# Kernel optimization log

Hardware: AMD Instinct MI355X
Metric: run time of the kernel (lower is better)

The kernel has to match this reference:

```python
import jax, jax.numpy as jnp
import numpy as np
from jax import lax


def _sobel_kernels(angle_deg, channel_n):
    dx = np.outer([1.0, 2.0, 1.0], [-1.0, 0.0, 1.0]) / 8.0
    dy = dx.T
    c = np.cos(angle_deg * np.pi / 180.0)
    s = np.sin(angle_deg * np.pi / 180.0)
    w1 = (c * dx - s * dy).astype(np.float32)
    w2 = (s * dx + c * dy).astype(np.float32)
    # depthwise kernels [C, 1, 3, 3] (OIHW with feature_group_count=C)
    k1 = jnp.tile(jnp.asarray(w1)[None, None], (channel_n, 1, 1, 1))
    k2 = jnp.tile(jnp.asarray(w2)[None, None], (channel_n, 1, 1, 1))
    return k1, k2


def _dwconv(x, k, groups):
    return lax.conv_general_dilated(
        x, k, window_strides=(1, 1), padding=[(1, 1), (1, 1)],
        feature_group_count=groups,
        dimension_numbers=('NCHW', 'OIHW', 'NCHW'))


def _maxpool3(x):
    # 3x3 max pool, stride 1, pad 1 over last two dims of NCHW
    return lax.reduce_window(x, -jnp.inf, lax.max,
                             (1, 1, 3, 3), (1, 1, 1, 1),
                             [(0, 0), (0, 0), (1, 1), (1, 1)])


def _alive(x_nchw):
    return _maxpool3(x_nchw[:, 3:4]) > 0.1


def _update(x, key, w0, b0, w1, wfr, k1, k2):
    # x: [B, H, W, C]  (torch does transpose(1,3) -> [B, C, W, H])
    xc = jnp.swapaxes(x, 1, 3)
    pre = _alive(xc)                               # [B,1,W,H] bool
    cn = xc.shape[1]
    y1 = _dwconv(xc, k1, cn)
    y2 = _dwconv(xc, k2, cn)
    dx = jnp.swapaxes(jnp.concatenate([xc, y1, y2], axis=1), 1, 3)  # [B,H,W,3C]
    fr = jax.nn.sigmoid(dx @ wfr.T) * jnp.swapaxes(pre, 1, 3)       # [B,H,W,1]
    log_fr = jnp.log(jnp.concatenate([fr, 1.0 - fr], axis=-1) + 1e-10)
    h = jax.nn.relu(dx @ w0.T + b0) @ w1.T                           # [B,H,W,C]
    # gumbel-softmax, tau=1, hard=True (straight-through)
    u = jax.random.uniform(key, log_fr.shape)
    g = -jnp.log(-jnp.log(u + 1e-20) + 1e-20)
    soft = jax.nn.softmax(log_fr + g, axis=-1)
    hard = jax.nn.one_hot(jnp.argmax(soft, axis=-1), 2, dtype=soft.dtype)
    update_grid = (hard + soft - lax.stop_gradient(soft))[..., 0:1]
    h = h * update_grid
    xc = xc + jnp.swapaxes(h, 1, 3)
    post = _alive(xc)
    xc = xc * (pre & post).astype(xc.dtype)
    return jnp.swapaxes(xc, 1, 3), fr[..., 0]


def setup_inputs() -> dict:
    key = jax.random.key(0)
    k = jax.random.split(key, 5)
    B, H, W, C, HID = 16, 128, 128, 16, 256
    return {
        'x': jax.random.uniform(k[0], (B, H, W, C), dtype=jnp.float32),
        'w0': jax.random.normal(k[1], (HID, 3 * C), dtype=jnp.float32) * 0.1,
        'b0': jax.random.normal(k[2], (HID,), dtype=jnp.float32) * 0.01,
        'w1': jax.random.normal(k[3], (C, HID), dtype=jnp.float32) * 0.1,
        'wfr': jax.random.normal(k[4], (1, 3 * C), dtype=jnp.float32) * 0.1,
        'steps': 4,
    }


def reference(x, w0, b0, w1, wfr, steps):
    angle = 0.0
    k1, k2 = _sobel_kernels(angle, x.shape[-1])
    keys = jax.random.split(jax.random.key(42), steps)

    def step(carry, key):
        xn, fr = _update(carry, key, w0, b0, w1, wfr, k1, k2)
        return xn, (xn, fr)

    _, (x_steps, fr_steps) = lax.scan(step, x, keys)
    return x_steps, fr_steps
```

## Files before the change

kernel.cpp:

```cpp
#include <hip/hip_runtime.h>
#include <cstdint>
#include <math.h>

#define HW2    16384
#define BHW    262144
#define XSLICE 4194304

__host__ __device__ static inline uint32_t rotl32(uint32_t v, int r) {
  return (v << r) | (v >> (32 - r));
}

__host__ __device__ static inline void tf2x32(uint32_t k0, uint32_t k1,
                                              uint32_t x0, uint32_t x1,
                                              uint32_t& o0, uint32_t& o1) {
  uint32_t ks2 = k0 ^ k1 ^ 0x1BD11BDAu;
  x0 += k0; x1 += k1;
#define TFR(r) { x0 += x1; x1 = rotl32(x1, (r)); x1 ^= x0; }
  TFR(13) TFR(15) TFR(26) TFR(6)   x0 += k1;  x1 += ks2 + 1u;
  TFR(17) TFR(29) TFR(16) TFR(24)  x0 += ks2; x1 += k0 + 2u;
  TFR(13) TFR(15) TFR(26) TFR(6)   x0 += k0;  x1 += k1 + 3u;
  TFR(17) TFR(29) TFR(16) TFR(24)  x0 += k1;  x1 += ks2 + 4u;
  TFR(13) TFR(15) TFR(26) TFR(6)   x0 += ks2; x1 += k0 + 5u;
#undef TFR
  o0 = x0; o1 = x1;
}

__device__ static inline float bits_to_unit(uint32_t bits) {
  return __uint_as_float((bits >> 9) | 0x3f800000u) - 1.0f;
}

__device__ static inline uint32_t rng_bits(uint32_t sk0, uint32_t sk1, uint32_t f) {
  uint32_t o0, o1;
  tf2x32(sk0, sk1, 0u, f, o0, o1);
  return o0 ^ o1;
}

__device__ static inline float sigmoidf_(float z) {
  if (z >= 0.f) { float e = expf(-z); return 1.f / (1.f + e); }
  float e = expf(z); return e / (1.f + e);
}

__device__ static inline void sobel_feat(const float* __restrict__ base,
                                         int hh, int ww, float* dxv, float& m3) {
#pragma unroll
  for (int c = 0; c < 48; ++c) dxv[c] = 0.f;
  m3 = -INFINITY;
#pragma unroll
  for (int dh = -1; dh <= 1; ++dh) {
    const int j = dh + 1;
    const int h2 = hh + dh;
    const bool hok = ((unsigned)h2 < 128u);
#pragma unroll
    for (int dw = -1; dw <= 1; ++dw) {
      const int i = dw + 1;
      const int w2 = ww + dw;
      float v[16];
      if (hok && ((unsigned)w2 < 128u)) {
        const float* s = base + (((h2 << 7) + w2) << 4);
#pragma unroll
        for (int c = 0; c < 16; c += 4) {
          float4 q = *(const float4*)(s + c);
          v[c] = q.x; v[c + 1] = q.y; v[c + 2] = q.z; v[c + 3] = q.w;
        }
        m3 = fmaxf(m3, v[3]);
      } else {
#pragma unroll
        for (int c = 0; c < 16; ++c) v[c] = 0.f;
      }
      const float smv[3] = {1.f, 2.f, 1.f};
      const float dfv[3] = {-1.f, 0.f, 1.f};
      const float c1 = smv[i] * dfv[j] * 0.125f;
      const float c2 = dfv[i] * smv[j] * 0.125f;
      if (dh == 0 && dw == 0) {
#pragma unroll
        for (int c = 0; c < 16; ++c) dxv[c] = v[c];
      }
      if (c1 != 0.f) {
#pragma unroll
        for (int c = 0; c < 16; ++c) dxv[16 + c] = fmaf(c1, v[c], dxv[16 + c]);
      }
      if (c2 != 0.f) {
#pragma unroll
        for (int c = 0; c < 16; ++c) dxv[32 + c] = fmaf(c2, v[c], dxv[32 + c]);
      }
    }
  }
}

__global__ __launch_bounds__(256, 2) void ca_step_a(
    const float* __restrict__ xin,
    const float* __restrict__ pw,
    const float* __restrict__ wfrg,
    float* __restrict__ xmid,
    float* __restrict__ ch3,
    float* __restrict__ premask,
    float* __restrict__ frout,
    uint32_t sk0, uint32_t sk1) {
  __shared__ float sw[128 * 68];

  const int tid = threadIdx.x;
  {
    const float4* src = (const float4*)pw;
    float4* dst = (float4*)sw;
    for (int i = tid; i < 2176; i += 256) dst[i] = src[i];
  }
  __syncthreads();

  const int p0  = blockIdx.x * 512 + tid;
  const int p1  = p0 + 256;
  const int b   = p0 >> 14;
  const int rem = p0 & 16383;
  const int hh0 = rem >> 7;
  const int ww0 = rem & 127;
  const int hh1 = hh0 + 2;

  const float* base = xin + ((size_t)b << 18);

  float dx0[48], dx1[48];
  float m30, m31;
  sobel_feat(base, hh0, ww0, dx0, m30);
  sobel_feat(base, hh1, ww0, dx1, m31);

  const bool pre0 = (m30 > 0.1f);
  const bool pre1 = (m31 > 0.1f);

  float z0 = 0.f, z1 = 0.f;
#pragma unroll
  for (int c = 0; c < 48; ++c) {
    z0 = fmaf(dx0[c], wfrg[c], z0);
    z1 = fmaf(dx1[c], wfrg[c], z1);
  }
  const float fr0 = pre0 ? sigmoidf_(z0) : 0.f;
  const float fr1 = pre1 ? sigmoidf_(z1) : 0.f;

  float upd0, upd1;
  {
    const float u0 = bits_to_unit(rng_bits(sk0, sk1, 2u * (uint32_t)p0));
    const float u1 = bits_to_unit(rng_bits(sk0, sk1, 2u * (uint32_t)p0 + 1u));
    const float d0 = logf(fr0 + 1e-10f) - logf(-logf(u0 + 1e-20f) + 1e-20f);
    const float d1 = logf(1.0f - fr0 + 1e-10f) - logf(-logf(u1 + 1e-20f) + 1e-20f);
    upd0 = (d0 >= d1) ? 1.f : 0.f;
  }
  {
    const float u0 = bits_to_unit(rng_bits(sk0, sk1, 2u * (uint32_t)p1));
    const float u1 = bits_to_unit(rng_bits(sk0, sk1, 2u * (uint32_t)p1 + 1u));
    const float d0 = logf(fr1 + 1e-10f) - logf(-logf(u0 + 1e-20f) + 1e-20f);
    const float d1 = logf(1.0f - fr1 + 1e-10f) - logf(-logf(u1 + 1e-20f) + 1e-20f);
    upd1 = (d0 >= d1) ? 1.f : 0.f;
  }

  float h0[16], h1[16];
#pragma unroll
  for (int c = 0; c < 16; ++c) { h0[c] = 0.f; h1[c] = 0.f; }

  for (int i = 0; i < 128; ++i) {
    const float* __restrict__ srow = pw + (size_t)(128 + i) * 68;
    float S[65];
#pragma unroll
    for (int q = 0; q < 65; ++q) S[q] = srow[q];

    {
      const float* row = sw + i * 68;
      float a00 = 0.f, a01 = 0.f, a10 = 0.f, a11 = 0.f;
#pragma unroll
      for (int ks = 0; ks < 6; ++ks) {
        const int k = ks * 8;
        const float4 wa = *(const float4*)(row + k);
        const float4 wb = *(const float4*)(row + k + 4);
        a00 = fmaf(wa.x, dx0[k + 0], a00); a01 = fmaf(wa.y, dx0[k + 1], a01);
        a00 = fmaf(wa.z, dx0[k + 2], a00); a01 = fmaf(wa.w, dx0[k + 3], a01);
        a00 = fmaf(wb.x, dx0[k + 4], a00); a01 = fmaf(wb.y, dx0[k + 5], a01);
        a00 = fmaf(wb.z, dx0[k + 6], a00); a01 = fmaf(wb.w, dx0[k + 7], a01);
        a10 = fmaf(wa.x, dx1[k + 0], a10); a11 = fmaf(wa.y, dx1[k + 1], a11);
        a10 = fmaf(wa.z, dx1[k + 2], a10); a11 = fmaf(wa.w, dx1[k + 3], a11);
        a10 = fmaf(wb.x, dx1[k + 4], a10); a11 = fmaf(wb.y, dx1[k + 5], a11);
        a10 = fmaf(wb.z, dx1[k + 6], a10); a11 = fmaf(wb.w, dx1[k + 7], a11);
      }
      const float bb = row[64];
      const float r0 = fmaxf(bb + (a00 + a01), 0.f);
      const float r1 = fmaxf(bb + (a10 + a11), 0.f);
#pragma unroll
      for (int c4 = 0; c4 < 4; ++c4) {
        const float4 q = *(const float4*)(row + 48 + (c4 << 2));
        const int c = c4 << 2;
        h0[c]     = fmaf(q.x, r0, h0[c]);     h1[c]     = fmaf(q.x, r1, h1[c]);
        h0[c + 1] = fmaf(q.y, r0, h0[c + 1]); h1[c + 1] = fmaf(q.y, r1, h1[c + 1]);
        h0[c + 2] = fmaf(q.z, r0, h0[c + 2]); h1[c + 2] = fmaf(q.z, r1, h1[c + 2]);
        h0[c + 3] = fmaf(q.w, r0, h0[c + 3]); h1[c + 3] = fmaf(q.w, r1, h1[c + 3]);
      }
    }

    {
      float a00 = 0.f, a01 = 0.f, a10 = 0.f, a11 = 0.f;
#pragma unroll
      for (int k = 0; k < 48; k += 2) {
        a00 = fmaf(S[k], dx0[k], a00);     a01 = fmaf(S[k + 1], dx0[k + 1], a01);
        a10 = fmaf(S[k], dx1[k], a10);     a11 = fmaf(S[k + 1], dx1[k + 1], a11);
      }
      const float bb = S[64];
      const float r0 = fmaxf(bb + (a00 + a01), 0.f);
      const float r1 = fmaxf(bb + (a10 + a11), 0.f);
#pragma unroll
      for (int c = 0; c < 16; ++c) {
        h0[c] = fmaf(S[48 + c], r0, h0[c]);
        h1[c] = fmaf(S[48 + c], r1, h1[c]);
      }
    }
  }

  float* dst0 = xmid + ((size_t)p0 << 4);
  float* dst1 = xmid + ((size_t)p1 << 4);
#pragma unroll
  for (int c = 0; c < 16; c += 4) {
    float4 q0, q1;
    q0.x = fmaf(upd0, h0[c],     dx0[c]);     q1.x = fmaf(upd1, h1[c],     dx1[c]);
    q0.y = fmaf(upd0, h0[c + 1], dx0[c + 1]); q1.y = fmaf(upd1, h1[c + 1], dx1[c + 1]);
    q0.z = fmaf(upd0, h0[c + 2], dx0[c + 2]); q1.z = fmaf(upd1, h1[c + 2], dx1[c + 2]);
    q0.w = fmaf(upd0, h0[c + 3], dx0[c + 3]); q1.w = fmaf(upd1, h1[c + 3], dx1[c + 3]);
    *(float4*)(dst0 + c) = q0;
    *(float4*)(dst1 + c) = q1;
  }
  ch3[p0]     = fmaf(upd0, h0[3], dx0[3]);
  ch3[p1]     = fmaf(upd1, h1[3], dx1[3]);
  premask[p0] = pre0 ? 1.f : 0.f;
  premask[p1] = pre1 ? 1.f : 0.f;
  frout[p0]   = fr0;
  frout[p1]   = fr1;
}

__global__ __launch_bounds__(256) void ca_step_b(
    float* __restrict__ xs, const float* __restrict__ ch3,
    const float* __restrict__ premask) {
  const int p   = blockIdx.x * 256 + threadIdx.x;
  const int b   = p >> 14;
  const int rem = p & 16383;
  const int hh  = rem >> 7;
  const int ww  = rem & 127;
  const float* cb = ch3 + (b << 14);
  float m = -INFINITY;
#pragma unroll
  for (int dh = -1; dh <= 1; ++dh) {
    const int h2 = hh + dh;
    if ((unsigned)h2 >= 128u) continue;
#pragma unroll
    for (int dw = -1; dw <= 1; ++dw) {
      const int w2 = ww + dw;
      if ((unsigned)w2 >= 128u) continue;
      m = fmaxf(m, cb[(h2 << 7) + w2]);
    }
  }
  const bool alive = (premask[p] != 0.f) && (m > 0.1f);
  if (!alive) {
    float4 z; z.x = 0.f; z.y = 0.f; z.z = 0.f; z.w = 0.f;
    float* dst = xs + ((size_t)p << 4);
    *(float4*)(dst)      = z;
    *(float4*)(dst + 4)  = z;
    *(float4*)(dst + 8)  = z;
    *(float4*)(dst + 12) = z;
  }
}

__global__ void pack_weights(const float* __restrict__ w0,
                             const float* __restrict__ b0,
                             const float* __restrict__ w1,
                             float* __restrict__ pw) {
  const int j = blockIdx.x * 256 + threadIdx.x;
  if (j < 256) {
    float* r = pw + j * 68;
#pragma unroll
    for (int k = 0; k < 48; ++k) r[k] = w0[j * 48 + k];
#pragma unroll
    for (int c = 0; c < 16; ++c) r[48 + c] = w1[c * 256 + j];
    r[64] = b0[j];
    r[65] = 0.f; r[66] = 0.f; r[67] = 0.f;
  }
}

extern "C" void kernel_launch(void* const* d_in, const int* in_sizes, int n_in,
                              void* d_out, int out_size, void* d_ws, size_t ws_size,
                              hipStream_t stream) {
  const float* x0  = (const float*)d_in[0];
  const float* w0  = (const float*)d_in[1];
  const float* b0  = (const float*)d_in[2];
  const float* w1  = (const float*)d_in[3];
  const float* wfr = (const float*)d_in[4];
  const int steps = 4;

  float* xsteps  = (float*)d_out;
  float* frsteps = xsteps + (size_t)steps * XSLICE;

  float* pw  = (float*)d_ws;
  float* ch3 = pw + 17408;
  float* pre = ch3 + BHW;

  uint32_t sk[4][2];
  for (int s = 0; s < steps; ++s)
    tf2x32(0u, 42u, 0u, (uint32_t)s, sk[s][0], sk[s][1]);

  pack_weights<<<1, 256, 0, stream>>>(w0, b0, w1, pw);
  for (int s = 0; s < steps; ++s) {
    const float* xin = (s == 0) ? x0 : (xsteps + (size_t)(s - 1) * XSLICE);
    float* xmid = xsteps + (size_t)s * XSLICE;
    ca_step_a<<<512, 256, 0, stream>>>(xin, pw, wfr, xmid, ch3, pre,
                                       frsteps + (size_t)s * BHW, sk[s][0], sk[s][1]);
    ca_step_b<<<1024, 256, 0, stream>>>(xmid, ch3, pre);
  }
}
```

Before: 462.8 us.

## Compact updating cells into a list and run the MLP only on them

Splits the step kernel into a gate kernel and an MLP kernel. The gate kernel computes the perception features, fire rate and Gumbel decision, writes the un-updated state, and appends the indices of updating cells to a list through an atomic counter. The MLP kernel then runs the hidden layer only over the compacted list, so cells with no update skip the 256-wide MLP. The price is an extra launch, recomputing Sobel features in the second kernel, gather-style scattered access, and nondeterministic list order from the atomics.

```diff
diff --git a/kernel.cpp b/kernel.cpp
--- a/kernel.cpp
+++ b/kernel.cpp
@@ -87,17 +87,67 @@
   }
 }
 
-__global__ __launch_bounds__(256, 2) void ca_step_a(
+__global__ __launch_bounds__(256) void ca_gate(
     const float* __restrict__ xin,
-    const float* __restrict__ pw,
     const float* __restrict__ wfrg,
     float* __restrict__ xmid,
     float* __restrict__ ch3,
     float* __restrict__ premask,
     float* __restrict__ frout,
+    int* __restrict__ list,
+    int* __restrict__ counter,
     uint32_t sk0, uint32_t sk1) {
+  const int p   = blockIdx.x * 256 + threadIdx.x;
+  const int b   = p >> 14;
+  const int rem = p & 16383;
+  const int hh  = rem >> 7;
+  const int ww  = rem & 127;
+
+  const float* base = xin + ((size_t)b << 18);
+  float dxv[48];
+  float m3;
+  sobel_feat(base, hh, ww, dxv, m3);
+  const bool pre = (m3 > 0.1f);
+
+  float z = 0.f;
+#pragma unroll
+  for (int c = 0; c < 48; ++c) z = fmaf(dxv[c], wfrg[c], z);
+  const float fr = pre ? sigmoidf_(z) : 0.f;
+
+  const float u0 = bits_to_unit(rng_bits(sk0, sk1, 2u * (uint32_t)p));
+  const float u1 = bits_to_unit(rng_bits(sk0, sk1, 2u * (uint32_t)p + 1u));
+  const float d0 = logf(fr + 1e-10f) - logf(-logf(u0 + 1e-20f) + 1e-20f);
+  const float d1 = logf(1.0f - fr + 1e-10f) - logf(-logf(u1 + 1e-20f) + 1e-20f);
+  const bool updb = (d0 >= d1);
+
+  float* dst = xmid + ((size_t)p << 4);
+#pragma unroll
+  for (int c = 0; c < 16; c += 4) {
+    float4 q;
+    q.x = dxv[c]; q.y = dxv[c + 1]; q.z = dxv[c + 2]; q.w = dxv[c + 3];
+    *(float4*)(dst + c) = q;
+  }
+  ch3[p]     = dxv[3];
+  premask[p] = pre ? 1.f : 0.f;
+  frout[p]   = fr;
+  if (updb) {
+    const int slot = atomicAdd(counter, 1);
+    list[slot] = p;
+  }
+}
+
+__global__ __launch_bounds__(256, 2) void ca_mlp(
+    const float* __restrict__ xin,
+    const float* __restrict__ pw,
+    const int* __restrict__ list,
+    const int* __restrict__ counter,
+    float* __restrict__ xmid,
+    float* __restrict__ ch3) {
+  const int count = *counter;
+  const int chunk = blockIdx.x * 512;
+  if (chunk >= count) return;
+
   __shared__ float sw[128 * 68];
-
   const int tid = threadIdx.x;
   {
     const float4* src = (const float4*)pw;
@@ -106,47 +156,22 @@
   }
   __syncthreads();
 
-  const int p0  = blockIdx.x * 512 + tid;
-  const int p1  = p0 + 256;
-  const int b   = p0 >> 14;
-  const int rem = p0 & 16383;
-  const int hh0 = rem >> 7;
-  const int ww0 = rem & 127;
-  const int hh1 = hh0 + 2;
-
-  const float* base = xin + ((size_t)b << 18);
+  const int e0 = chunk + tid;
+  const int e1 = e0 + 256;
+  const bool v0 = (e0 < count);
+  const bool v1 = (e1 < count);
+  const int p0 = v0 ? list[e0] : list[0];
+  const int p1 = v1 ? list[e1] : list[0];
 
   float dx0[48], dx1[48];
   float m30, m31;
-  sobel_feat(base, hh0, ww0, dx0, m30);
-  sobel_feat(base, hh1, ww0, dx1, m31);
-
-  const bool pre0 = (m30 > 0.1f);
-  const bool pre1 = (m31 > 0.1f);
-
-  float z0 = 0.f, z1 = 0.f;
-#pragma unroll
-  for (int c = 0; c < 48; ++c) {
-    z0 = fmaf(dx0[c], wfrg[c], z0);
-    z1 = fmaf(dx1[c], wfrg[c], z1);
-  }
-  const float fr0 = pre0 ? sigmoidf_(z0) : 0.f;
-  const float fr1 = pre1 ? sigmoidf_(z1) : 0.f;
-
-  float upd0, upd1;
   {
-    const float u0 = bits_to_unit(rng_bits(sk0, sk1, 2u * (uint32_t)p0));
-    const float u1 = bits_to_unit(rng_bits(sk0, sk1, 2u * (uint32_t)p0 + 1u));
-    const float d0 = logf(fr0 + 1e-10f) - logf(-logf(u0 + 1e-20f) + 1e-20f);
-    const float d1 = logf(1.0f - fr0 + 1e-10f) - logf(-logf(u1 + 1e-20f) + 1e-20f);
-    upd0 = (d0 >= d1) ? 1.f : 0.f;
+    const int b = p0 >> 14, rem = p0 & 16383;
+    sobel_feat(xin + ((size_t)b << 18), rem >> 7, rem & 127, dx0, m30);
   }
   {
-    const float u0 = bits_to_unit(rng_bits(sk0, sk1, 2u * (uint32_t)p1));
-    const float u1 = bits_to_unit(rng_bits(sk0, sk1, 2u * (uint32_t)p1 + 1u));
-    const float d0 = logf(fr1 + 1e-10f) - logf(-logf(u0 + 1e-20f) + 1e-20f);
-    const float d1 = logf(1.0f - fr1 + 1e-10f) - logf(-logf(u1 + 1e-20f) + 1e-20f);
-    upd1 = (d0 >= d1) ? 1.f : 0.f;
+    const int b = p1 >> 14, rem = p1 & 16383;
+    sobel_feat(xin + ((size_t)b << 18), rem >> 7, rem & 127, dx1, m31);
   }
 
   float h0[16], h1[16];
@@ -208,24 +233,32 @@
     }
   }
 
-  float* dst0 = xmid + ((size_t)p0 << 4);
-  float* dst1 = xmid + ((size_t)p1 << 4);
-#pragma unroll
-  for (int c = 0; c < 16; c += 4) {
-    float4 q0, q1;
-    q0.x = fmaf(upd0, h0[c],     dx0[c]);     q1.x = fmaf(upd1, h1[c],     dx1[c]);
-    q0.y = fmaf(upd0, h0[c + 1], dx0[c + 1]); q1.y = fmaf(upd1, h1[c + 1], dx1[c + 1]);
-    q0.z = fmaf(upd0, h0[c + 2], dx0[c + 2]); q1.z = fmaf(upd1, h1[c + 2], dx1[c + 2]);
-    q0.w = fmaf(upd0, h0[c + 3], dx0[c + 3]); q1.w = fmaf(upd1, h1[c + 3], dx1[c + 3]);
-    *(float4*)(dst0 + c) = q0;
-    *(float4*)(dst1 + c) = q1;
-  }
-  ch3[p0]     = fmaf(upd0, h0[3], dx0[3]);
-  ch3[p1]     = fmaf(upd1, h1[3], dx1[3]);
-  premask[p0] = pre0 ? 1.f : 0.f;
-  premask[p1] = pre1 ? 1.f : 0.f;
-  frout[p0]   = fr0;
-  frout[p1]   = fr1;
+  if (v0) {
+    float* dst = xmid + ((size_t)p0 << 4);
+#pragma unroll
+    for (int c = 0; c < 16; c += 4) {
+      float4 q;
+      q.x = dx0[c]     + h0[c];
+      q.y = dx0[c + 1] + h0[c + 1];
+      q.z = dx0[c + 2] + h0[c + 2];
+      q.w = dx0[c + 3] + h0[c + 3];
+      *(float4*)(dst + c) = q;
+    }
+    ch3[p0] = dx0[3] + h0[3];
+  }
+  if (v1) {
+    float* dst = xmid + ((size_t)p1 << 4);
+#pragma unroll
+    for (int c = 0; c < 16; c += 4) {
+      float4 q;
+      q.x = dx1[c]     + h1[c];
+      q.y = dx1[c + 1] + h1[c + 1];
+      q.z = dx1[c + 2] + h1[c + 2];
+      q.w = dx1[c + 3] + h1[c + 3];
+      *(float4*)(dst + c) = q;
+    }
+    ch3[p1] = dx1[3] + h1[3];
+  }
 }
 
 __global__ __launch_bounds__(256) void ca_step_b(
@@ -263,7 +296,8 @@
 __global__ void pack_weights(const float* __restrict__ w0,
                              const float* __restrict__ b0,
                              const float* __restrict__ w1,
-                             float* __restrict__ pw) {
+                             float* __restrict__ pw,
+                             int* __restrict__ counters) {
   const int j = blockIdx.x * 256 + threadIdx.x;
   if (j < 256) {
     float* r = pw + j * 68;
@@ -274,6 +308,7 @@
     r[64] = b0[j];
     r[65] = 0.f; r[66] = 0.f; r[67] = 0.f;
   }
+  if (j < 4) counters[j] = 0;
 }
 
 extern "C" void kernel_launch(void* const* d_in, const int* in_sizes, int n_in,
@@ -289,20 +324,24 @@
   float* xsteps  = (float*)d_out;
   float* frsteps = xsteps + (size_t)steps * XSLICE;
 
-  float* pw  = (float*)d_ws;
-  float* ch3 = pw + 17408;
-  float* pre = ch3 + BHW;
+  float* pw   = (float*)d_ws;
+  float* ch3  = pw + 17408;
+  float* pre  = ch3 + BHW;
+  int*   list = (int*)(pre + BHW);
+  int*   cnts = list + BHW;
 
   uint32_t sk[4][2];
   for (int s = 0; s < steps; ++s)
     tf2x32(0u, 42u, 0u, (uint32_t)s, sk[s][0], sk[s][1]);
 
-  pack_weights<<<1, 256, 0, stream>>>(w0, b0, w1, pw);
+  pack_weights<<<1, 256, 0, stream>>>(w0, b0, w1, pw, cnts);
   for (int s = 0; s < steps; ++s) {
     const float* xin = (s == 0) ? x0 : (xsteps + (size_t)(s - 1) * XSLICE);
     float* xmid = xsteps + (size_t)s * XSLICE;
-    ca_step_a<<<512, 256, 0, stream>>>(xin, pw, wfr, xmid, ch3, pre,
-                                       frsteps + (size_t)s * BHW, sk[s][0], sk[s][1]);
+    ca_gate<<<1024, 256, 0, stream>>>(xin, wfr, xmid, ch3, pre,
+                                      frsteps + (size_t)s * BHW, list, cnts + s,
+                                      sk[s][0], sk[s][1]);
+    ca_mlp<<<512, 256, 0, stream>>>(xin, pw, list, cnts + s, xmid, ch3);
     ca_step_b<<<1024, 256, 0, stream>>>(xmid, ch3, pre);
   }
 }
```

New measurement: 617.6 us. +33.4%, slower.
